# Kernel tuning notes

Measured on AMD Instinct MI355X. Metric: run time of the kernel, lower is better.

## Reference

```python
import jax, jax.numpy as jnp
import numpy as np

B, S, HID, NH = 4, 8192, 1024, 32
DH = HID // NH  # 32 == NH, required by the module's broadcast multiply


def setup_inputs() -> dict:
    key = jax.random.key(0)
    ks = jax.random.split(key, 9)
    scale = 1.0 / np.sqrt(HID)
    return {
        "query": jax.random.normal(ks[0], (B, S, HID), jnp.float32),
        "key": jax.random.normal(ks[1], (B, S, HID), jnp.float32),
        "value": jax.random.normal(ks[2], (B, S, HID), jnp.float32),
        "Wq": jax.random.normal(ks[3], (HID, HID), jnp.float32) * scale,
        "bq": jnp.zeros((HID,), jnp.float32),
        "Wk": jax.random.normal(ks[4], (HID, HID), jnp.float32) * scale,
        "bk": jnp.zeros((HID,), jnp.float32),
        "Wv": jax.random.normal(ks[5], (HID, HID), jnp.float32) * scale,
        "bv": jnp.zeros((HID,), jnp.float32),
    }


def reference(query, key, value, Wq, bq, Wk, bk, Wv, bv):
    # Linear projections (torch Linear: x @ W.T + b)
    q = (query @ Wq.T + bq).reshape(B, S, NH, DH)
    k = (key @ Wk.T + bk).reshape(B, S, NH, DH)
    v = (value @ Wv.T + bv).reshape(B, S, NH, DH)
    # NOTE: source does NOT transpose heads to a batch dim, so matmul
    # contracts head_dim per-token: scores[b,s,h,t] over heads h,t.
    scores = jnp.einsum('bshd,bstd->bsht', q, k) / jnp.sqrt(jnp.float32(HID))
    scores = jax.nn.softmax(scores, axis=-1)  # softmax over heads axis t
    # Dropout is identity in inference mode.
    # Elementwise broadcast multiply [B,S,H,H] * [B,S,H,DH] (H == DH)
    out = scores * v
    return out.reshape(B, S, HID)
```

## Files before the change

kernel.cpp:

```cpp
#include <hip/hip_runtime.h>
#include <hip/hip_bf16.h>


typedef __attribute__((ext_vector_type(8))) short bf16x8;
typedef __attribute__((ext_vector_type(4))) float f32x4;

#define HID 1024

#define GLOAD_LDS16(gp, lp)                                                   \
  __builtin_amdgcn_global_load_lds(                                           \
      (const __attribute__((address_space(1))) void*)(gp),                    \
      (__attribute__((address_space(3))) void*)(lp), 16, 0, 0)

__device__ __forceinline__ unsigned short f2bf(float f) {
  unsigned int u = __builtin_bit_cast(unsigned int, f);
  u += 0x7FFFu + ((u >> 16) & 1u);
  return (unsigned short)(u >> 16);
}
__device__ __forceinline__ float bf2f(unsigned short h) {
  unsigned int u = (unsigned int)h << 16;
  return __builtin_bit_cast(float, u);
}

__device__ __forceinline__ bf16x8 cvt8(f32x4 a, f32x4 b) {
  union { unsigned int u[4]; bf16x8 v; } r;
  asm("v_cvt_pk_bf16_f32 %0, %1, %2" : "=v"(r.u[0]) : "v"(a[0]), "v"(a[1]));
  asm("v_cvt_pk_bf16_f32 %0, %1, %2" : "=v"(r.u[1]) : "v"(a[2]), "v"(a[3]));
  asm("v_cvt_pk_bf16_f32 %0, %1, %2" : "=v"(r.u[2]) : "v"(b[0]), "v"(b[1]));
  asm("v_cvt_pk_bf16_f32 %0, %1, %2" : "=v"(r.u[3]) : "v"(b[2]), "v"(b[3]));
  return r.v;
}

__global__ __launch_bounds__(256)
void convw_kernel(const float* __restrict__ src, unsigned short* __restrict__ dst) {
  const int i = blockIdx.x * 256 + threadIdx.x;
  const f32x4 a = ((const f32x4*)src)[i * 2];
  const f32x4 b = ((const f32x4*)src)[i * 2 + 1];
  ((bf16x8*)dst)[i] = cvt8(a, b);
}

template<int MODE>
__global__ __launch_bounds__(256, 3)
void gemm_bf(const float* __restrict__ X, const unsigned short* __restrict__ Wb,
             const float* __restrict__ bias, void* outp,
             const unsigned short* __restrict__ pbf) {
  const int bid = blockIdx.x;
  const int L = (bid & 7) * 256 + (bid >> 3);
  const int m0 = (L >> 3) * 128;
  const int n0 = (L & 7) * 128;
  const int tid = threadIdx.x;
  const int lane = tid & 63;
  const int wid = tid >> 6;
  const int wm = (wid >> 1) << 6;
  const int wn = (wid & 1) << 6;
  const int lo = lane & 15, grp = lane >> 4;

  __shared__ __align__(16) unsigned char lds[2][24576];

  size_t asrc[4]; unsigned int adst[4];
#pragma unroll
  for (int q = 0; q < 4; ++q) {
    const int g = q * 256 + tid;
    const int row = g >> 3, s = g & 7;
    asrc[q] = (size_t)(m0 + row) * 4096 + (size_t)(((s ^ (row & 7)) << 4));
    adst[q] = g * 16;
  }
  size_t bsrc[2]; unsigned int bdst[2];
#pragma unroll
  for (int q = 0; q < 2; ++q) {
    const int g = q * 256 + tid;
    const int row = g >> 2, s = g & 3;
    bsrc[q] = (size_t)(n0 + row) * 2048 + (size_t)(((s ^ ((row >> 1) & 3)) << 4));
    bdst[q] = 16384u + g * 16;
  }
  const char* Xc = (const char*)X;
  const char* Wc = (const char*)Wb;

  auto stage = [&](int b, int kt) {
    const size_t ka = (size_t)kt * 128;
    const size_t kb = (size_t)kt * 64;
#pragma unroll
    for (int q = 0; q < 4; ++q) GLOAD_LDS16(Xc + asrc[q] + ka, &lds[b][adst[q]]);
#pragma unroll
    for (int q = 0; q < 2; ++q) GLOAD_LDS16(Wc + bsrc[q] + kb, &lds[b][bdst[q]]);
  };

  int aoff[4][2], boff[4];
#pragma unroll
  for (int f = 0; f < 4; ++f) {
    const int ra = wm + f * 16 + lo;
    aoff[f][0] = ra * 128 + ((((2 * grp)     ^ (ra & 7)) << 4));
    aoff[f][1] = ra * 128 + ((((2 * grp + 1) ^ (ra & 7)) << 4));
    const int rb = wn + f * 16 + lo;
    boff[f] = 16384 + rb * 64 + ((grp ^ ((rb >> 1) & 3)) << 4);
  }

  f32x4 acc[4][4] = {};
  auto compute = [&](int b) {
    bf16x8 af[4], bfm[4];
#pragma unroll
    for (int f = 0; f < 4; ++f) {
      const f32x4 a0 = *(const f32x4*)&lds[b][aoff[f][0]];
      const f32x4 a1 = *(const f32x4*)&lds[b][aoff[f][1]];
      af[f] = cvt8(a0, a1);
      bfm[f] = *(const bf16x8*)&lds[b][boff[f]];
    }
#pragma unroll
    for (int fm = 0; fm < 4; ++fm)
#pragma unroll
      for (int fn = 0; fn < 4; ++fn)
        acc[fm][fn] = __builtin_amdgcn_mfma_f32_16x16x32_bf16(
            af[fm], bfm[fn], acc[fm][fn], 0, 0, 0);
  };

  stage(0, 0);
#pragma unroll 1
  for (int kt = 0; kt < 32; ++kt) {
    if (kt < 31) {
      stage((kt + 1) & 1, kt + 1);
      __builtin_amdgcn_sched_barrier(0);
      asm volatile("s_waitcnt vmcnt(6)" ::: "memory");
    } else {
      __builtin_amdgcn_sched_barrier(0);
      asm volatile("s_waitcnt vmcnt(0)" ::: "memory");
    }
    __builtin_amdgcn_s_barrier();
    __builtin_amdgcn_sched_barrier(0);
    compute(kt & 1);
    __builtin_amdgcn_sched_barrier(0);
    __builtin_amdgcn_s_barrier();
    __builtin_amdgcn_sched_barrier(0);
  }

  unsigned char* eb = &lds[0][0];
  const unsigned char* ebc = eb;
  if (MODE == 2) {
    float* of = (float*)outp;
#pragma unroll
    for (int fm = 0; fm < 4; ++fm) {
      const int row = m0 + wm + fm * 16 + grp * 4;
#pragma unroll
      for (int fn = 0; fn < 4; ++fn) {
        const int col = n0 + wn + fn * 16 + lo;
        const float bc = bias[col];
#pragma unroll
        for (int j = 0; j < 4; ++j) {
          const size_t idx = (size_t)(row + j) * 1024 + col;
          of[idx] = bf2f(pbf[idx]) * (acc[fm][fn][j] + bc);
        }
      }
    }
  } else {
    const float scale = (MODE == 0) ? 0.03125f : 1.0f;
#pragma unroll
    for (int fm = 0; fm < 4; ++fm) {
#pragma unroll
      for (int fn = 0; fn < 4; ++fn) {
        const int colL = wn + fn * 16 + lo;
        const float bc = bias[n0 + colL];
#pragma unroll
        for (int j = 0; j < 4; ++j) {
          const int rowL = wm + fm * 16 + grp * 4 + j;
          const int byte = rowL * 256 + ((colL * 2) ^ ((rowL & 7) << 5));
          *(unsigned short*)&eb[byte] = f2bf((acc[fm][fn][j] + bc) * scale);
        }
      }
    }
    __syncthreads();
    unsigned short* ob = (unsigned short*)outp;
    const int half = (MODE == 1) ? 1024 : 0;
#pragma unroll
    for (int p = 0; p < 8; ++p) {
      const int r = p * 16 + (tid >> 4);
      const int c0 = (tid & 15) * 8;
      const uint4 v = *(const uint4*)&ebc[r * 256 + ((c0 * 2) ^ ((r & 7) << 5))];
      *(uint4*)&ob[(size_t)(m0 + r) * 2048 + half + n0 + c0] = v;
    }
  }
}

template<int MODE>
__global__ __launch_bounds__(256, 2)
void gemm_fb(const float* __restrict__ X, const float* __restrict__ W,
             const float* __restrict__ bias, void* outp,
             const unsigned short* __restrict__ pbf, int use_ws) {
  const int bid = blockIdx.x;
  const int L = (bid & 7) * 256 + (bid >> 3);
  const int m0 = (L >> 3) * 128;
  const int n0 = (L & 7) * 128;
  const int tid = threadIdx.x;
  const int lane = tid & 63;
  const int wid = tid >> 6;
  const int wm = (wid >> 1) << 6;
  const int wn = (wid & 1) << 6;
  const int lo = lane & 15, grp = lane >> 4;
  __shared__ __align__(16) unsigned char lds[2][32768];
  const int srow = tid >> 3;
  const int sk8  = tid & 7;
  const float* Ag = X + (size_t)(m0 + srow) * HID + sk8 * 8;
  const float* Bg = W + (size_t)(n0 + srow) * HID + sk8 * 8;
  f32x4 la[4][2], lb[4][2];
  auto gload = [&](int k0) {
#pragma unroll
    for (int rr = 0; rr < 4; ++rr) {
      const float* ap = Ag + (size_t)(rr * 32) * HID + k0;
      const float* bp = Bg + (size_t)(rr * 32) * HID + k0;
      la[rr][0] = *(const f32x4*)(ap); la[rr][1] = *(const f32x4*)(ap + 4);
      lb[rr][0] = *(const f32x4*)(bp); lb[rr][1] = *(const f32x4*)(bp + 4);
    }
  };
  auto cvtwrite = [&](int b) {
#pragma unroll
    for (int rr = 0; rr < 4; ++rr) {
      const int row = srow + rr * 32;
      const int adr = row * 128 + ((sk8 ^ (row & 7)) << 4);
      *(bf16x8*)&lds[b][adr]         = cvt8(la[rr][0], la[rr][1]);
      *(bf16x8*)&lds[b][16384 + adr] = cvt8(lb[rr][0], lb[rr][1]);
    }
  };
  f32x4 acc[4][4] = {};
  auto compute = [&](int b) {
#pragma unroll
    for (int kk = 0; kk < 2; ++kk) {
      const int slot = kk * 4 + grp;
      bf16x8 af[4], bfm[4];
#pragma unroll
      for (int f = 0; f < 4; ++f) {
        const int ra = wm + f * 16 + lo;
        const int rb = wn + f * 16 + lo;
        af[f]  = *(const bf16x8*)&lds[b][ra * 128 + ((slot ^ (ra & 7)) << 4)];
        bfm[f] = *(const bf16x8*)&lds[b][16384 + rb * 128 + ((slot ^ (rb & 7)) << 4)];
      }
#pragma unroll
      for (int fm = 0; fm < 4; ++fm)
#pragma unroll
        for (int fn = 0; fn < 4; ++fn)
          acc[fm][fn] = __builtin_amdgcn_mfma_f32_16x16x32_bf16(
              af[fm], bfm[fn], acc[fm][fn], 0, 0, 0);
    }
  };
  gload(0); cvtwrite(0); gload(64);
  __builtin_amdgcn_sched_barrier(0);
  asm volatile("s_waitcnt lgkmcnt(0)" ::: "memory");
  __builtin_amdgcn_s_barrier();
  __builtin_amdgcn_sched_barrier(0);
#pragma unroll 1
  for (int kt = 0; kt < 16; ++kt) {
    compute(kt & 1);
    if (kt < 15) {
      cvtwrite((kt + 1) & 1);
      if (kt < 14) gload((kt + 2) * 64);
    }
    __builtin_amdgcn_sched_barrier(0);
    asm volatile("s_waitcnt lgkmcnt(0)" ::: "memory");
    __builtin_amdgcn_s_barrier();
    __builtin_amdgcn_sched_barrier(0);
  }
  unsigned char* eb = &lds[0][0];
  const unsigned char* ebc = eb;
  if (MODE == 2) {
    float* of = (float*)outp;
#pragma unroll
    for (int fm = 0; fm < 4; ++fm) {
      const int row = m0 + wm + fm * 16 + grp * 4;
#pragma unroll
      for (int fn = 0; fn < 4; ++fn) {
        const int col = n0 + wn + fn * 16 + lo;
        const float bc = bias[col];
#pragma unroll
        for (int j = 0; j < 4; ++j) {
          const size_t idx = (size_t)(row + j) * 1024 + col;
          const float p = use_ws ? bf2f(pbf[idx]) : of[idx];
          of[idx] = p * (acc[fm][fn][j] + bc);
        }
      }
    }
  } else {
    const float scale = (MODE == 0) ? 0.03125f : 1.0f;
#pragma unroll
    for (int fm = 0; fm < 4; ++fm) {
#pragma unroll
      for (int fn = 0; fn < 4; ++fn) {
        const int colL = wn + fn * 16 + lo;
        const float bc = bias[n0 + colL];
#pragma unroll
        for (int j = 0; j < 4; ++j) {
          const int rowL = wm + fm * 16 + grp * 4 + j;
          const int byte = rowL * 256 + ((colL * 2) ^ ((rowL & 7) << 5));
          *(unsigned short*)&eb[byte] = f2bf((acc[fm][fn][j] + bc) * scale);
        }
      }
    }
    __syncthreads();
    unsigned short* ob = (unsigned short*)outp;
    const int half = (MODE == 1) ? 1024 : 0;
#pragma unroll
    for (int p = 0; p < 8; ++p) {
      const int r = p * 16 + (tid >> 4);
      const int c0 = (tid & 15) * 8;
      const uint4 v = *(const uint4*)&ebc[r * 256 + ((c0 * 2) ^ ((r & 7) << 5))];
      *(uint4*)&ob[(size_t)(m0 + r) * 2048 + half + n0 + c0] = v;
    }
  }
}

template<int PMODE>
__global__ __launch_bounds__(256)
void attn_kernel(float* __restrict__ dout, unsigned short* __restrict__ wsp) {
  const int wid = threadIdx.x >> 6;
  const int lane = threadIdx.x & 63;
  const int token = blockIdx.x * 4 + wid;
  const int lo = lane & 15, grp = lane >> 4;
  const unsigned short* qk = (const unsigned short*)dout + (size_t)token * 2048;
  const int base = lo * 32 + grp * 8;

  bf16x8 a0 = *(const bf16x8*)(qk + base);
  bf16x8 a1 = *(const bf16x8*)(qk + 512 + base);
  bf16x8 b0 = *(const bf16x8*)(qk + 1024 + base);
  bf16x8 b1 = *(const bf16x8*)(qk + 1536 + base);
  asm volatile("s_waitcnt vmcnt(0)" ::: "memory");

  const f32x4 z = {0.f, 0.f, 0.f, 0.f};
  f32x4 s[2][2];
  s[0][0] = __builtin_amdgcn_mfma_f32_16x16x32_bf16(a0, b0, z, 0, 0, 0);
  s[0][1] = __builtin_amdgcn_mfma_f32_16x16x32_bf16(a0, b1, z, 0, 0, 0);
  s[1][0] = __builtin_amdgcn_mfma_f32_16x16x32_bf16(a1, b0, z, 0, 0, 0);
  s[1][1] = __builtin_amdgcn_mfma_f32_16x16x32_bf16(a1, b1, z, 0, 0, 0);

  float* od = dout + (size_t)token * 1024;
  unsigned short* ob = wsp + (size_t)token * 1024;
#pragma unroll
  for (int rt = 0; rt < 2; ++rt) {
#pragma unroll
    for (int j = 0; j < 4; ++j) {
      const float v0 = s[rt][0][j], v1 = s[rt][1][j];
      float m = fmaxf(v0, v1);
#pragma unroll
      for (int msk = 1; msk < 16; msk <<= 1) m = fmaxf(m, __shfl_xor(m, msk, 64));
      const float e0 = __expf(v0 - m), e1 = __expf(v1 - m);
      float ssum = e0 + e1;
#pragma unroll
      for (int msk = 1; msk < 16; msk <<= 1) ssum += __shfl_xor(ssum, msk, 64);
      const float inv = 1.0f / ssum;
      const int h = rt * 16 + grp * 4 + j;
      if (PMODE == 0) {
        od[h * 32 + lo]      = e0 * inv;
        od[h * 32 + 16 + lo] = e1 * inv;
      } else {
        ob[h * 32 + lo]      = f2bf(e0 * inv);
        ob[h * 32 + 16 + lo] = f2bf(e1 * inv);
      }
    }
  }
}

extern "C" void kernel_launch(void* const* d_in, const int* in_sizes, int n_in,
                              void* d_out, int out_size, void* d_ws, size_t ws_size,
                              hipStream_t stream) {
  const float* query = (const float*)d_in[0];
  const float* key   = (const float*)d_in[1];
  const float* value = (const float*)d_in[2];
  const float* Wq    = (const float*)d_in[3];
  const float* bq    = (const float*)d_in[4];
  const float* Wk    = (const float*)d_in[5];
  const float* bk    = (const float*)d_in[6];
  const float* Wv    = (const float*)d_in[7];
  const float* bv    = (const float*)d_in[8];

  const size_t P_BYTES = (size_t)32768 * 1024 * 2;
  const size_t W_BYTES = (size_t)1024 * 1024 * 2;
  unsigned short* pbf = (unsigned short*)d_ws;
  unsigned short* Wqb = (unsigned short*)((char*)d_ws + P_BYTES);
  unsigned short* Wkb = Wqb + (W_BYTES / 2);
  unsigned short* Wvb = Wkb + (W_BYTES / 2);

  if (ws_size >= P_BYTES + 3 * W_BYTES) {
    convw_kernel<<<dim3(512), dim3(256), 0, stream>>>(Wq, Wqb);
    convw_kernel<<<dim3(512), dim3(256), 0, stream>>>(Wk, Wkb);
    convw_kernel<<<dim3(512), dim3(256), 0, stream>>>(Wv, Wvb);
    gemm_bf<0><<<dim3(2048), dim3(256), 0, stream>>>(query, Wqb, bq, d_out, pbf);
    gemm_bf<1><<<dim3(2048), dim3(256), 0, stream>>>(key,   Wkb, bk, d_out, pbf);
    attn_kernel<1><<<dim3(8192), dim3(256), 0, stream>>>((float*)d_out, pbf);
    gemm_bf<2><<<dim3(2048), dim3(256), 0, stream>>>(value, Wvb, bv, d_out, pbf);
  } else {
    const int use_ws = (ws_size >= P_BYTES) ? 1 : 0;
    gemm_fb<0><<<dim3(2048), dim3(256), 0, stream>>>(query, Wq, bq, d_out, nullptr, 0);
    gemm_fb<1><<<dim3(2048), dim3(256), 0, stream>>>(key,   Wk, bk, d_out, nullptr, 0);
    if (use_ws)
      attn_kernel<1><<<dim3(8192), dim3(256), 0, stream>>>((float*)d_out, pbf);
    else
      attn_kernel<0><<<dim3(8192), dim3(256), 0, stream>>>((float*)d_out, nullptr);
    gemm_fb<2><<<dim3(2048), dim3(256), 0, stream>>>(value, Wv, bv, d_out, pbf, use_ws);
  }
}
```

Measured before the change: 423.1 us.

## Replace 128x128 projection GEMM with 256x256-tile kernel converting A to bf16 once

Replaces the 128x128-tile, 256-thread projection GEMM with a 256x256-tile, 512-thread kernel. The fp32 activations are now loaded through registers and converted to bf16 once before being written to LDS, instead of copied as fp32 into LDS and converted on every fragment read. The larger tile halves global re-reads of X and W per output element, and MFMA sections are wrapped in setprio. In exchange it uses 128KB of LDS with occupancy of one block per CU, runs only 512 blocks, and splits the epilogue into two LDS-staged halves.

```diff
diff --git a/kernel.cpp b/kernel.cpp
--- a/kernel.cpp
+++ b/kernel.cpp
@@ -40,104 +40,113 @@
 }
 
 template<int MODE>
-__global__ __launch_bounds__(256, 3)
-void gemm_bf(const float* __restrict__ X, const unsigned short* __restrict__ Wb,
+__global__ __launch_bounds__(512, 1)
+void gemm256(const float* __restrict__ X, const unsigned short* __restrict__ Wb,
              const float* __restrict__ bias, void* outp,
              const unsigned short* __restrict__ pbf) {
   const int bid = blockIdx.x;
-  const int L = (bid & 7) * 256 + (bid >> 3);
-  const int m0 = (L >> 3) * 128;
-  const int n0 = (L & 7) * 128;
+  const int L = (bid & 7) * 64 + (bid >> 3);
+  const int m0 = (L >> 2) * 256;
+  const int n0 = (L & 3) * 256;
   const int tid = threadIdx.x;
   const int lane = tid & 63;
   const int wid = tid >> 6;
-  const int wm = (wid >> 1) << 6;
-  const int wn = (wid & 1) << 6;
+  const int wm = (wid >> 2) * 128;
+  const int wn = (wid & 3) * 64;
   const int lo = lane & 15, grp = lane >> 4;
 
-  __shared__ __align__(16) unsigned char lds[2][24576];
-
-  size_t asrc[4]; unsigned int adst[4];
-#pragma unroll
-  for (int q = 0; q < 4; ++q) {
-    const int g = q * 256 + tid;
-    const int row = g >> 3, s = g & 7;
-    asrc[q] = (size_t)(m0 + row) * 4096 + (size_t)(((s ^ (row & 7)) << 4));
-    adst[q] = g * 16;
-  }
-  size_t bsrc[2]; unsigned int bdst[2];
-#pragma unroll
-  for (int q = 0; q < 2; ++q) {
-    const int g = q * 256 + tid;
-    const int row = g >> 2, s = g & 3;
-    bsrc[q] = (size_t)(n0 + row) * 2048 + (size_t)(((s ^ ((row >> 1) & 3)) << 4));
-    bdst[q] = 16384u + g * 16;
-  }
-  const char* Xc = (const char*)X;
+  __shared__ __align__(16) unsigned char lds[2][65536];
+
+  const int srow = tid >> 1;
+  const int sh   = tid & 1;
+  const float* Ag = X + (size_t)(m0 + srow) * HID + sh * 32;
+  f32x4 ar[8];
+  auto aload = [&](int kt) {
+    const float* p = Ag + kt * 64;
+#pragma unroll
+    for (int i = 0; i < 8; ++i) ar[i] = *(const f32x4*)(p + i * 4);
+  };
+  auto awrite = [&](int b) {
+#pragma unroll
+    for (int i = 0; i < 4; ++i) {
+      const int s = sh * 4 + i;
+      *(bf16x8*)&lds[b][srow * 128 + ((s ^ (srow & 7)) << 4)] =
+          cvt8(ar[2 * i], ar[2 * i + 1]);
+    }
+  };
   const char* Wc = (const char*)Wb;
-
-  auto stage = [&](int b, int kt) {
-    const size_t ka = (size_t)kt * 128;
-    const size_t kb = (size_t)kt * 64;
-#pragma unroll
-    for (int q = 0; q < 4; ++q) GLOAD_LDS16(Xc + asrc[q] + ka, &lds[b][adst[q]]);
-#pragma unroll
-    for (int q = 0; q < 2; ++q) GLOAD_LDS16(Wc + bsrc[q] + kb, &lds[b][bdst[q]]);
-  };
-
-  int aoff[4][2], boff[4];
-#pragma unroll
-  for (int f = 0; f < 4; ++f) {
-    const int ra = wm + f * 16 + lo;
-    aoff[f][0] = ra * 128 + ((((2 * grp)     ^ (ra & 7)) << 4));
-    aoff[f][1] = ra * 128 + ((((2 * grp + 1) ^ (ra & 7)) << 4));
-    const int rb = wn + f * 16 + lo;
-    boff[f] = 16384 + rb * 64 + ((grp ^ ((rb >> 1) & 3)) << 4);
-  }
-
-  f32x4 acc[4][4] = {};
+  size_t bsrc[4];
+#pragma unroll
+  for (int i = 0; i < 4; ++i) {
+    const int g = tid + i * 512;
+    const int row = g >> 3, j = g & 7;
+    bsrc[i] = (size_t)(n0 + row) * 2048 + (size_t)((j ^ (row & 7)) << 4);
+  }
+  auto bstage = [&](int b, int kt) {
+    const size_t kb = (size_t)kt * 128;
+#pragma unroll
+    for (int i = 0; i < 4; ++i)
+      GLOAD_LDS16(Wc + bsrc[i] + kb, &lds[b][32768 + tid * 16 + i * 8192]);
+  };
+
+  f32x4 acc[8][4] = {};
   auto compute = [&](int b) {
-    bf16x8 af[4], bfm[4];
-#pragma unroll
-    for (int f = 0; f < 4; ++f) {
-      const f32x4 a0 = *(const f32x4*)&lds[b][aoff[f][0]];
-      const f32x4 a1 = *(const f32x4*)&lds[b][aoff[f][1]];
-      af[f] = cvt8(a0, a1);
-      bfm[f] = *(const bf16x8*)&lds[b][boff[f]];
-    }
-#pragma unroll
-    for (int fm = 0; fm < 4; ++fm)
-#pragma unroll
-      for (int fn = 0; fn < 4; ++fn)
-        acc[fm][fn] = __builtin_amdgcn_mfma_f32_16x16x32_bf16(
-            af[fm], bfm[fn], acc[fm][fn], 0, 0, 0);
-  };
-
-  stage(0, 0);
+#pragma unroll
+    for (int kk = 0; kk < 2; ++kk) {
+      const int s = kk * 4 + grp;
+      bf16x8 af[8], bfm[4];
+#pragma unroll
+      for (int f = 0; f < 8; ++f) {
+        const int ra = wm + f * 16 + lo;
+        af[f] = *(const bf16x8*)&lds[b][ra * 128 + ((s ^ (ra & 7)) << 4)];
+      }
+#pragma unroll
+      for (int g = 0; g < 4; ++g) {
+        const int rb = wn + g * 16 + lo;
+        bfm[g] = *(const bf16x8*)&lds[b][32768 + rb * 128 + ((s ^ (rb & 7)) << 4)];
+      }
+      __builtin_amdgcn_s_setprio(1);
+#pragma unroll
+      for (int fm = 0; fm < 8; ++fm)
+#pragma unroll
+        for (int fn = 0; fn < 4; ++fn)
+          acc[fm][fn] = __builtin_amdgcn_mfma_f32_16x16x32_bf16(
+              af[fm], bfm[fn], acc[fm][fn], 0, 0, 0);
+      __builtin_amdgcn_s_setprio(0);
+    }
+  };
+
+  aload(0);
+  awrite(0);
+  bstage(0, 0);
+  aload(1);
+  __builtin_amdgcn_sched_barrier(0);
+  asm volatile("s_waitcnt vmcnt(8)" ::: "memory");
+  asm volatile("s_waitcnt lgkmcnt(0)" ::: "memory");
+  __builtin_amdgcn_s_barrier();
+  __builtin_amdgcn_sched_barrier(0);
+
 #pragma unroll 1
-  for (int kt = 0; kt < 32; ++kt) {
-    if (kt < 31) {
-      stage((kt + 1) & 1, kt + 1);
-      __builtin_amdgcn_sched_barrier(0);
-      asm volatile("s_waitcnt vmcnt(6)" ::: "memory");
-    } else {
-      __builtin_amdgcn_sched_barrier(0);
-      asm volatile("s_waitcnt vmcnt(0)" ::: "memory");
-    }
+  for (int kt = 0; kt < 16; ++kt) {
+    const int cur = kt & 1;
+    if (kt < 15) {
+      awrite(cur ^ 1);
+      bstage(cur ^ 1, kt + 1);
+      if (kt < 14) aload(kt + 2);
+    }
+    compute(cur);
+    __builtin_amdgcn_sched_barrier(0);
+    if (kt < 14) asm volatile("s_waitcnt vmcnt(8)" ::: "memory");
+    else         asm volatile("s_waitcnt vmcnt(0)" ::: "memory");
+    asm volatile("s_waitcnt lgkmcnt(0)" ::: "memory");
     __builtin_amdgcn_s_barrier();
     __builtin_amdgcn_sched_barrier(0);
-    compute(kt & 1);
-    __builtin_amdgcn_sched_barrier(0);
-    __builtin_amdgcn_s_barrier();
-    __builtin_amdgcn_sched_barrier(0);
-  }
-
-  unsigned char* eb = &lds[0][0];
-  const unsigned char* ebc = eb;
+  }
+
   if (MODE == 2) {
     float* of = (float*)outp;
 #pragma unroll
-    for (int fm = 0; fm < 4; ++fm) {
+    for (int fm = 0; fm < 8; ++fm) {
       const int row = m0 + wm + fm * 16 + grp * 4;
 #pragma unroll
       for (int fn = 0; fn < 4; ++fn) {
@@ -152,29 +161,40 @@
     }
   } else {
     const float scale = (MODE == 0) ? 0.03125f : 1.0f;
-#pragma unroll
-    for (int fm = 0; fm < 4; ++fm) {
-#pragma unroll
-      for (int fn = 0; fn < 4; ++fn) {
-        const int colL = wn + fn * 16 + lo;
-        const float bc = bias[n0 + colL];
-#pragma unroll
-        for (int j = 0; j < 4; ++j) {
-          const int rowL = wm + fm * 16 + grp * 4 + j;
-          const int byte = rowL * 256 + ((colL * 2) ^ ((rowL & 7) << 5));
-          *(unsigned short*)&eb[byte] = f2bf((acc[fm][fn][j] + bc) * scale);
-        }
-      }
-    }
-    __syncthreads();
+    unsigned short* lds16 = (unsigned short*)&lds[0][0];
     unsigned short* ob = (unsigned short*)outp;
     const int half = (MODE == 1) ? 1024 : 0;
-#pragma unroll
-    for (int p = 0; p < 8; ++p) {
-      const int r = p * 16 + (tid >> 4);
-      const int c0 = (tid & 15) * 8;
-      const uint4 v = *(const uint4*)&ebc[r * 256 + ((c0 * 2) ^ ((r & 7) << 5))];
-      *(uint4*)&ob[(size_t)(m0 + r) * 2048 + half + n0 + c0] = v;
+    float bcol[4];
+#pragma unroll
+    for (int fn = 0; fn < 4; ++fn) bcol[fn] = bias[n0 + wn + fn * 16 + lo];
+#pragma unroll 1
+    for (int h = 0; h < 2; ++h) {
+      if ((wid >> 2) == h) {
+#pragma unroll
+        for (int fm = 0; fm < 8; ++fm)
+#pragma unroll
+          for (int fn = 0; fn < 4; ++fn)
+#pragma unroll
+            for (int j = 0; j < 4; ++j) {
+              const int rl = fm * 16 + grp * 4 + j;
+              const int col = wn + fn * 16 + lo;
+              lds16[rl * 256 + (col ^ (grp << 4))] =
+                  f2bf((acc[fm][fn][j] + bcol[fn]) * scale);
+            }
+      }
+      __syncthreads();
+      {
+        const int row = tid >> 2;
+        const int c0 = (tid & 3) * 64;
+        const int x = ((row >> 2) & 3) << 4;
+#pragma unroll
+        for (int q = 0; q < 8; ++q) {
+          const int cg = c0 + q * 8;
+          const uint4 v = *(const uint4*)&lds16[row * 256 + (cg ^ x)];
+          *(uint4*)&ob[(size_t)(m0 + h * 128 + row) * 2048 + half + n0 + cg] = v;
+        }
+      }
+      __syncthreads();
     }
   }
 }
@@ -378,10 +398,10 @@
     convw_kernel<<<dim3(512), dim3(256), 0, stream>>>(Wq, Wqb);
     convw_kernel<<<dim3(512), dim3(256), 0, stream>>>(Wk, Wkb);
     convw_kernel<<<dim3(512), dim3(256), 0, stream>>>(Wv, Wvb);
-    gemm_bf<0><<<dim3(2048), dim3(256), 0, stream>>>(query, Wqb, bq, d_out, pbf);
-    gemm_bf<1><<<dim3(2048), dim3(256), 0, stream>>>(key,   Wkb, bk, d_out, pbf);
+    gemm256<0><<<dim3(512), dim3(512), 0, stream>>>(query, Wqb, bq, d_out, pbf);
+    gemm256<1><<<dim3(512), dim3(512), 0, stream>>>(key,   Wkb, bk, d_out, pbf);
     attn_kernel<1><<<dim3(8192), dim3(256), 0, stream>>>((float*)d_out, pbf);
-    gemm_bf<2><<<dim3(2048), dim3(256), 0, stream>>>(value, Wvb, bv, d_out, pbf);
+    gemm256<2><<<dim3(512), dim3(512), 0, stream>>>(value, Wvb, bv, d_out, pbf);
   } else {
     const int use_ws = (ws_size >= P_BYTES) ? 1 : 0;
     gemm_fb<0><<<dim3(2048), dim3(256), 0, stream>>>(query, Wq, bq, d_out, nullptr, 0);
```

Result: slower. 446.2 us (+5.5%).
